# Kernel tuning notes

Hardware: AMD Instinct MI355X
Metric: run time of the kernel (lower is better)

Reference implementation:

```python
import math
import jax, jax.numpy as jnp
import numpy as np

DIM, NHEAD, TOPK = 1024, 16, 64
DK = DIM // NHEAD
HIDDEN = int(DIM * 8.0)
EPS = 1e-5


def setup_inputs() -> dict:
    key = jax.random.key(0)
    ks = jax.random.split(key, 12)
    B, T = 2, 2048
    s = 0.02
    return {
        "x": jax.random.normal(ks[0], (B, T, DIM), jnp.float32),
        "ln1_g": jnp.ones((DIM,), jnp.float32),
        "ln1_b": jnp.zeros((DIM,), jnp.float32),
        "w_qkv": jax.random.normal(ks[1], (DIM, 3 * DIM), jnp.float32) * s,
        "alpha_head": jnp.zeros((NHEAD,), jnp.float32),
        "w_out": jax.random.normal(ks[2], (DIM, DIM), jnp.float32) * s,
        "ln2_g": jnp.ones((DIM,), jnp.float32),
        "ln2_b": jnp.zeros((DIM,), jnp.float32),
        "w1": jax.random.normal(ks[3], (DIM, HIDDEN), jnp.float32) * s,
        "b1": jnp.zeros((HIDDEN,), jnp.float32),
        "w2": jax.random.normal(ks[4], (HIDDEN, DIM), jnp.float32) * s,
        "b2": jnp.zeros((DIM,), jnp.float32),
        "alpha": jnp.float32(0.5),
    }


def _layernorm(x, g, b):
    mu = jnp.mean(x, axis=-1, keepdims=True)
    var = jnp.var(x, axis=-1, keepdims=True)
    return (x - mu) * jax.lax.rsqrt(var + EPS) * g + b


def _adaptive_sparse_attn(xn, w_qkv, alpha_head, w_out):
    B, T, C = xn.shape
    qkv = xn @ w_qkv  # [B,T,3C]
    q, k, v = jnp.split(qkv, 3, axis=-1)
    def heads(t):
        return t.reshape(B, T, NHEAD, DK).transpose(0, 2, 1, 3)  # [B,H,T,dk]
    q, k, v = heads(q), heads(k), heads(v)
    attn = jnp.einsum("bhqd,bhkd->bhqk", q, k) / math.sqrt(DK)  # [B,H,T,T]
    dense = jnp.einsum("bhqk,bhkd->bhqd", jax.nn.softmax(attn, axis=-1), v)
    # top-k sparse branch (TOPK < T)
    _, idx = jax.lax.top_k(attn, TOPK)  # [B,H,T,TOPK]
    M = B * NHEAD * T
    keep = jnp.zeros((M, T), bool).at[jnp.arange(M)[:, None], idx.reshape(M, TOPK)].set(True)
    keep = keep.reshape(B, NHEAD, T, T)
    attn_sp = jnp.where(keep, attn, jnp.float32(-1e9))
    sparse = jnp.einsum("bhqk,bhkd->bhqd", jax.nn.softmax(attn_sp, axis=-1), v)
    gate = jax.nn.sigmoid(alpha_head)[None, :, None, None]
    out = gate * dense + (1.0 - gate) * sparse  # [B,H,T,dk]
    out = out.transpose(0, 2, 1, 3).reshape(B, T, C)
    return out @ w_out


def reference(x, ln1_g, ln1_b, w_qkv, alpha_head, w_out, ln2_g, ln2_b, w1, b1, w2, b2, alpha):
    # attention sub-block with learned residual scale alpha
    x = x + alpha * _adaptive_sparse_attn(_layernorm(x, ln1_g, ln1_b), w_qkv, alpha_head, w_out)
    # FFN (dropout in eval mode -> identity); exact GELU as torch default
    h = jax.nn.gelu(_layernorm(x, ln2_g, ln2_b) @ w1 + b1, approximate=False)
    x = x + alpha * (h @ w2 + b2)
    return x
```

## Files before the change

kernel.cpp:

```cpp
#include <hip/hip_runtime.h>
#include <math.h>

#define DIMC 1024
#define NHEADC 16
#define DKC 64
#define HIDC 8192
#define TSEQ 2048
#define BATCH 2
#define NROWS (BATCH*TSEQ)
#define EPSF 1e-5f

typedef __attribute__((ext_vector_type(8))) short short8;
typedef __attribute__((ext_vector_type(4))) float floatx4;

__device__ __forceinline__ ushort f2bf(float f){
  unsigned u = __float_as_uint(f);
  unsigned r = (u + 0x7FFFu + ((u>>16)&1u)) >> 16;
  return (ushort)r;
}
__device__ __forceinline__ float bf2f(ushort u){
  return __uint_as_float(((unsigned)u)<<16);
}
__device__ __forceinline__ floatx4 mfma16(short8 a, short8 b, floatx4 c){
  return __builtin_amdgcn_mfma_f32_16x16x32_bf16(a, b, c, 0, 0, 0);
}
__device__ __forceinline__ void gld_lds16(const void* g, void* l){
  __builtin_amdgcn_global_load_lds((const __attribute__((address_space(1))) unsigned*)g,
                                   (__attribute__((address_space(3))) unsigned*)l, 16, 0, 0);
}
__device__ __forceinline__ float wred_add(float v){
  #pragma unroll
  for (int o = 32; o > 0; o >>= 1) v += __shfl_xor(v, o, 64);
  return v;
}
__device__ __forceinline__ float wred_max(float v){
  #pragma unroll
  for (int o = 32; o > 0; o >>= 1) v = fmaxf(v, __shfl_xor(v, o, 64));
  return v;
}

__global__ __launch_bounds__(256)
void wconv_t(const float* __restrict__ W, ushort* __restrict__ WT, int K, int N)
{
  __shared__ float tile[32][33];
  const int t = threadIdx.x, tx = t & 31, ty = t >> 5;
  const int n0 = blockIdx.x * 32, k0 = blockIdx.y * 32;
  #pragma unroll
  for (int r = 0; r < 4; ++r)
    tile[ty + r*8][tx] = W[(size_t)(k0 + ty + r*8) * N + n0 + tx];
  __syncthreads();
  #pragma unroll
  for (int r = 0; r < 4; ++r)
    WT[(size_t)(n0 + ty + r*8) * K + k0 + tx] = f2bf(tile[tx][ty + r*8]);
}

__global__ __launch_bounds__(256)
void vtrans(const ushort* __restrict__ qkv, ushort* __restrict__ vT)
{
  const int d = threadIdx.x & 63, tp = threadIdx.x >> 6;
  const int bh = blockIdx.y; const int h = bh & 15, b = bh >> 4;
  const int t0 = blockIdx.x * 32 + tp * 8;
  const ushort* src = qkv + ((size_t)(b*TSEQ) + t0) * (3*DIMC) + 2*DIMC + h*DKC + d;
  ushort tmp[8];
  #pragma unroll
  for (int k = 0; k < 8; ++k) tmp[k] = src[(size_t)k * (3*DIMC)];
  *(short8*)&vT[((size_t)bh*DKC + d)*TSEQ + t0] = *(const short8*)tmp;
}

__global__ __launch_bounds__(256)
void ln_bf16(const float* __restrict__ x, const float* __restrict__ g,
             const float* __restrict__ b, ushort* __restrict__ y)
{
  __shared__ float red[8];
  const int row = blockIdx.x;
  const float* xr = x + (size_t)row * DIMC;
  const int c = threadIdx.x * 4;
  float4 v = *(const float4*)&xr[c];
  float s  = v.x + v.y + v.z + v.w;
  float ss = v.x*v.x + v.y*v.y + v.z*v.z + v.w*v.w;
  s = wred_add(s); ss = wred_add(ss);
  const int warp = threadIdx.x >> 6, lane = threadIdx.x & 63;
  if (lane == 0) { red[warp] = s; red[4+warp] = ss; }
  __syncthreads();
  s  = red[0] + red[1] + red[2] + red[3];
  ss = red[4] + red[5] + red[6] + red[7];
  const float mu  = s  * (1.f/DIMC);
  const float var = ss * (1.f/DIMC) - mu*mu;
  const float rr  = rsqrtf(var + EPSF);
  const float4 gv = *(const float4*)&g[c];
  const float4 bv = *(const float4*)&b[c];
  ushort4 o;
  o.x = f2bf((v.x-mu)*rr*gv.x + bv.x);
  o.y = f2bf((v.y-mu)*rr*gv.y + bv.y);
  o.z = f2bf((v.z-mu)*rr*gv.z + bv.z);
  o.w = f2bf((v.w-mu)*rr*gv.w + bv.w);
  *(ushort4*)&y[(size_t)row*DIMC + c] = o;
}

#define M_PLAIN 0
#define M_RES 1
#define M_BIAS_GELU 2
#define M_BIAS_RES 3

template<int MODE>
__global__ __launch_bounds__(256)
void gemm_bf16(const ushort* __restrict__ A, const ushort* __restrict__ BT,
               void* __restrict__ Cout, const int M, const int N, const int K,
               const float* __restrict__ bias, const float* __restrict__ res,
               const float* __restrict__ alphap)
{
  __shared__ __align__(16) ushort Al[4][128][8];
  __shared__ __align__(16) ushort Bl[4][128][8];
  const int t = threadIdx.x;
  const int lane = t & 63, warp = t >> 6;
  const int quad = lane >> 4, l16 = lane & 15;
  const int m0 = (warp & 1) * 64, n0 = (warp >> 1) * 64;
  const size_t row0 = (size_t)blockIdx.y * 128;
  const size_t col0 = (size_t)blockIdx.x * 128;

  const int c0 = t, c1 = t + 256;
  const int ar0 = c0 & 127, as0 = c0 >> 7;
  const int ar1 = c1 & 127, as1 = c1 >> 7;
  const ushort* pa0 = A  + (row0 + ar0) * (size_t)K + as0 * 8;
  const ushort* pa1 = A  + (row0 + ar1) * (size_t)K + as1 * 8;
  const ushort* pb0 = BT + (col0 + ar0) * (size_t)K + as0 * 8;
  const ushort* pb1 = BT + (col0 + ar1) * (size_t)K + as1 * 8;
  ushort* la0 = &Al[as0][ar0][0];
  ushort* la1 = &Al[as1][ar1][0];
  ushort* lb0 = &Bl[as0][ar0][0];
  ushort* lb1 = &Bl[as1][ar1][0];

  floatx4 acc[4][4];
  const floatx4 zf = {0.f, 0.f, 0.f, 0.f};
  #pragma unroll
  for (int i = 0; i < 4; ++i)
    #pragma unroll
    for (int j = 0; j < 4; ++j) acc[i][j] = zf;

  for (int k0 = 0; k0 < K; k0 += 32) {
    gld_lds16(pa0 + k0, la0);
    gld_lds16(pa1 + k0, la1);
    gld_lds16(pb0 + k0, lb0);
    gld_lds16(pb1 + k0, lb1);
    __syncthreads();
    short8 af[4], bfr[4];
    #pragma unroll
    for (int i = 0; i < 4; ++i) {
      af[i]  = *(const short8*)&Al[quad][m0 + i*16 + l16][0];
      bfr[i] = *(const short8*)&Bl[quad][n0 + i*16 + l16][0];
    }
    #pragma unroll
    for (int mt = 0; mt < 4; ++mt)
      #pragma unroll
      for (int nt = 0; nt < 4; ++nt)
        acc[mt][nt] = mfma16(af[mt], bfr[nt], acc[mt][nt]);
    __syncthreads();
  }

  float alpha = 0.f;
  if (MODE == M_RES || MODE == M_BIAS_RES) alpha = alphap[0];
  #pragma unroll
  for (int nt = 0; nt < 4; ++nt) {
    const size_t col = col0 + n0 + nt*16 + l16;
    float bv = 0.f;
    if (MODE == M_BIAS_GELU || MODE == M_BIAS_RES) bv = bias[col];
    #pragma unroll
    for (int mt = 0; mt < 4; ++mt) {
      const size_t r0 = row0 + m0 + mt*16 + quad*4;
      #pragma unroll
      for (int reg = 0; reg < 4; ++reg) {
        float v = acc[mt][nt][reg];
        if (MODE == M_BIAS_GELU || MODE == M_BIAS_RES) v += bv;
        if (MODE == M_BIAS_GELU) v = 0.5f*v*(1.f + erff(v*0.70710678118654752f));
        if (MODE == M_RES || MODE == M_BIAS_RES) v = res[(r0+reg)*(size_t)N + col] + alpha*v;
        if (MODE == M_PLAIN || MODE == M_BIAS_GELU)
          ((ushort*)Cout)[(r0+reg)*(size_t)N + col] = f2bf(v);
        else
          ((float*)Cout)[(r0+reg)*(size_t)N + col] = v;
      }
    }
  }
}

__device__ __forceinline__ int swzf(int q){ return ((q>>2) ^ q) & 7; }
__device__ __forceinline__ int sidx(int q, int j){
  return (q << 11) + ((((j >> 3) ^ swzf(q)) << 3) | (j & 7));
}

__global__ __launch_bounds__(512, 4)
void attn_mfma(const ushort* __restrict__ qkv, const ushort* __restrict__ vT,
               const float* __restrict__ alpha_head, ushort* __restrict__ att)
{
  __shared__ __align__(16) ushort S[16*2048];
  __shared__ float Ored[4][16*17];
  const int t = threadIdx.x;
  const int lane = t & 63, warp = t >> 6;
  const int quad = lane >> 4, l16 = lane & 15;
  const int blk = blockIdx.x;
  const int bh  = blk >> 7;
  const int q0  = (blk & 127) << 4;
  const int h = bh & (NHEADC-1), b = bh >> 4;
  const size_t rowbase = (size_t)b * TSEQ;
  const floatx4 zf = {0.f, 0.f, 0.f, 0.f};

  const ushort* Qp = qkv + (rowbase + q0 + l16) * (size_t)(3*DIMC) + h*DKC + quad*8;
  const short8 aq0 = *(const short8*)Qp;
  const short8 aq1 = *(const short8*)(Qp + 32);

  const int j0w = warp * 256;
  #pragma unroll 2
  for (int jt = 0; jt < 16; ++jt) {
    const int j = j0w + jt*16;
    const ushort* Kp = qkv + (rowbase + j + l16) * (size_t)(3*DIMC) + DIMC + h*DKC + quad*8;
    const short8 kb0 = *(const short8*)Kp;
    const short8 kb1 = *(const short8*)(Kp + 32);
    floatx4 c = mfma16(aq0, kb0, zf);
    c = mfma16(aq1, kb1, c);
    #pragma unroll
    for (int r = 0; r < 4; ++r)
      S[sidx(quad*4 + r, j + l16)] = f2bf(c[r] * 0.125f);
  }
  __syncthreads();

  const float L2E = 1.4426950408889634f;
  const float gate = 1.f / (1.f + __expf(-alpha_head[h]));
  for (int rr = 0; rr < 2; ++rr) {
    const int q = warp*2 + rr;
    const int sbase = q << 11;
    const int swq = swzf(q);
    unsigned key[32]; float ev[32];
    float mx = -3.0e38f;
    #pragma unroll
    for (int p = 0; p < 16; ++p) {
      const int j = 2*lane + 128*p;
      const int g = (j >> 3) ^ swq;
      const unsigned pr = *(const unsigned*)&S[sbase + (g << 3) + (j & 7)];
      const unsigned u0 = pr & 0xFFFFu, u1 = pr >> 16;
      key[2*p]   = (u0 & 0x8000u) ? ((~u0) & 0xFFFFu) : (u0 | 0x8000u);
      key[2*p+1] = (u1 & 0x8000u) ? ((~u1) & 0xFFFFu) : (u1 | 0x8000u);
      const float v0 = __uint_as_float(pr << 16);
      const float v1 = __uint_as_float(pr & 0xFFFF0000u);
      ev[2*p] = v0; ev[2*p+1] = v1;
      mx = fmaxf(mx, fmaxf(v0, v1));
    }
    mx = wred_max(mx);
    const float nc = -mx * L2E;
    float sum_all = 0.f;
    #pragma unroll
    for (int i = 0; i < 32; ++i) { ev[i] = exp2f(fmaf(ev[i], L2E, nc)); sum_all += ev[i]; }
    sum_all = wred_add(sum_all);

    unsigned prefix = 0u;
    for (int bit = 15; bit >= 0; --bit) {
      const unsigned cand = prefix | (1u << bit);
      int c = 0;
      #pragma unroll
      for (int i = 0; i < 32; ++i)
        c += __popcll(__ballot(key[i] >= cand));
      if (c >= 64) prefix = cand;
    }
    unsigned inmask = 0u;
    float sum_sp = 0.f;
    int c_gt = 0;
    #pragma unroll
    for (int i = 0; i < 32; ++i) {
      const bool gbit = key[i] > prefix;
      c_gt += __popcll(__ballot(gbit));
      if (gbit) { inmask |= (1u << i); sum_sp += ev[i]; }
    }
    const int need_eq = 64 - c_gt;
    int eqb = 0;
    const unsigned long long below = (1ULL << lane) - 1ULL;
    for (int p = 0; p < 16; ++p) {
      const bool e0 = (key[2*p]   == prefix);
      const bool e1 = (key[2*p+1] == prefix);
      const unsigned long long m0 = __ballot(e0);
      const unsigned long long m1 = __ballot(e1);
      if (m0 | m1) {
        const int r0 = eqb + __popcll(m0 & below) + __popcll(m1 & below);
        const int r1 = r0 + (e0 ? 1 : 0);
        if (e0 && r0 < need_eq) { inmask |= (1u << (2*p));   sum_sp += ev[2*p]; }
        if (e1 && r1 < need_eq) { inmask |= (1u << (2*p+1)); sum_sp += ev[2*p+1]; }
        eqb += __popcll(m0) + __popcll(m1);
      }
    }
    sum_sp = wred_add(sum_sp);

    const float cd  = gate / sum_all;
    const float cdc = cd + (1.f - gate) / sum_sp;
    #pragma unroll
    for (int p = 0; p < 16; ++p) {
      const float w0 = ev[2*p]   * (((inmask >> (2*p))   & 1u) ? cdc : cd);
      const float w1 = ev[2*p+1] * (((inmask >> (2*p+1)) & 1u) ? cdc : cd);
      const int j = 2*lane + 128*p;
      const int g = (j >> 3) ^ swq;
      *(unsigned*)&S[sbase + (g << 3) + (j & 7)] =
          (unsigned)f2bf(w0) | ((unsigned)f2bf(w1) << 16);
    }
  }
  __syncthreads();

  const int n0  = (warp & 3) * 16;
  const int kt0 = (warp >> 2) * 32;
  floatx4 o = zf, o2 = zf;
  const ushort* Vb = vT + ((size_t)bh*DKC + n0 + l16) * TSEQ + quad*8;
  #pragma unroll 2
  for (int tt = 0; tt < 32; tt += 2) {
    const int kt = kt0 + tt;
    const short8 a0 = *(const short8*)&S[sidx(l16, kt*32 + quad*8)];
    const short8 vb0 = *(const short8*)(Vb + (size_t)kt*32);
    const short8 a1 = *(const short8*)&S[sidx(l16, (kt+1)*32 + quad*8)];
    const short8 vb1 = *(const short8*)(Vb + (size_t)(kt+1)*32);
    o  = mfma16(a0, vb0, o);
    o2 = mfma16(a1, vb1, o2);
  }
  o = o + o2;
  if (warp >= 4) {
    #pragma unroll
    for (int r = 0; r < 4; ++r) Ored[warp-4][(quad*4+r)*17 + l16] = o[r];
  }
  __syncthreads();
  if (warp < 4) {
    #pragma unroll
    for (int r = 0; r < 4; ++r) {
      const float v = o[r] + Ored[warp][(quad*4+r)*17 + l16];
      att[(rowbase + q0 + quad*4 + r) * (size_t)DIMC + h*DKC + n0 + l16] = f2bf(v);
    }
  }
}

extern "C" void kernel_launch(void* const* d_in, const int* in_sizes, int n_in,
                              void* d_out, int out_size, void* d_ws, size_t ws_size,
                              hipStream_t stream)
{
  const float* x          = (const float*)d_in[0];
  const float* ln1_g      = (const float*)d_in[1];
  const float* ln1_b      = (const float*)d_in[2];
  const float* w_qkv      = (const float*)d_in[3];
  const float* alpha_head = (const float*)d_in[4];
  const float* w_out      = (const float*)d_in[5];
  const float* ln2_g      = (const float*)d_in[6];
  const float* ln2_b      = (const float*)d_in[7];
  const float* w1         = (const float*)d_in[8];
  const float* b1         = (const float*)d_in[9];
  const float* w2         = (const float*)d_in[10];
  const float* b2         = (const float*)d_in[11];
  const float* alphap     = (const float*)d_in[12];
  float* out = (float*)d_out;

  char* ws = (char*)d_ws;
  ushort* wT_qkv = (ushort*)(ws);
  ushort* wT_out = (ushort*)(ws + 6291456);
  ushort* wT_1   = (ushort*)(ws + 8388608);
  ushort* wT_2   = (ushort*)(ws + 25165824);
  ushort* xn     = (ushort*)(ws + 41943040);
  ushort* qkv    = (ushort*)(ws + 50331648);
  ushort* attb   = (ushort*)(ws + 75497472);
  float*  x2     = (float*) (ws + 83886080);
  ushort* hbuf   = (ushort*)(ws + 100663296);
  ushort* vT     = (ushort*)(ws + 167772160);

  wconv_t<<<dim3(3072/32, 1024/32), 256, 0, stream>>>(w_qkv, wT_qkv, 1024, 3072);
  wconv_t<<<dim3(1024/32, 1024/32), 256, 0, stream>>>(w_out, wT_out, 1024, 1024);
  wconv_t<<<dim3(8192/32, 1024/32), 256, 0, stream>>>(w1,    wT_1,   1024, 8192);
  wconv_t<<<dim3(1024/32, 8192/32), 256, 0, stream>>>(w2,    wT_2,   8192, 1024);

  ln_bf16<<<NROWS, 256, 0, stream>>>(x, ln1_g, ln1_b, xn);
  gemm_bf16<M_PLAIN><<<dim3(3*DIMC/128, NROWS/128), 256, 0, stream>>>(
      xn, wT_qkv, qkv, NROWS, 3*DIMC, DIMC, nullptr, nullptr, nullptr);
  vtrans<<<dim3(64, 32), 256, 0, stream>>>(qkv, vT);
  attn_mfma<<<4096, 512, 0, stream>>>(qkv, vT, alpha_head, attb);
  gemm_bf16<M_RES><<<dim3(DIMC/128, NROWS/128), 256, 0, stream>>>(
      attb, wT_out, x2, NROWS, DIMC, DIMC, nullptr, x, alphap);
  ln_bf16<<<NROWS, 256, 0, stream>>>(x2, ln2_g, ln2_b, xn);
  gemm_bf16<M_BIAS_GELU><<<dim3(HIDC/128, NROWS/128), 256, 0, stream>>>(
      xn, wT_1, hbuf, NROWS, HIDC, DIMC, b1, nullptr, nullptr);
  gemm_bf16<M_BIAS_RES><<<dim3(DIMC/128, NROWS/128), 256, 0, stream>>>(
      hbuf, wT_2, out, NROWS, DIMC, HIDC, b2, x2, alphap);
}
```

Baseline: 1.018 ms.

## Double attention block to 1024 threads, one query row per warp

Widens the attention block from 8 to 16 warps so each warp computes half as many score tiles, runs the softmax/top-k selection on a single query row instead of two, and covers a quarter of the keys in the PV product. Partial outputs from the four key quarters are reduced through a larger shared buffer. The 1/sqrt(dk) scale is moved out of the score store and folded into the exp2 constant, so scores are stored unscaled in bf16, which slightly changes rounding. The cost is a 1024-thread block with tighter register limits per thread and one more level of partial-sum reduction.

```diff
diff --git a/kernel.cpp b/kernel.cpp
--- a/kernel.cpp
+++ b/kernel.cpp
@@ -17,9 +17,6 @@
   unsigned u = __float_as_uint(f);
   unsigned r = (u + 0x7FFFu + ((u>>16)&1u)) >> 16;
   return (ushort)r;
-}
-__device__ __forceinline__ float bf2f(ushort u){
-  return __uint_as_float(((unsigned)u)<<16);
 }
 __device__ __forceinline__ floatx4 mfma16(short8 a, short8 b, floatx4 c){
   return __builtin_amdgcn_mfma_f32_16x16x32_bf16(a, b, c, 0, 0, 0);
@@ -187,12 +184,12 @@
   return (q << 11) + ((((j >> 3) ^ swzf(q)) << 3) | (j & 7));
 }
 
-__global__ __launch_bounds__(512, 4)
+__global__ __launch_bounds__(1024, 8)
 void attn_mfma(const ushort* __restrict__ qkv, const ushort* __restrict__ vT,
                const float* __restrict__ alpha_head, ushort* __restrict__ att)
 {
   __shared__ __align__(16) ushort S[16*2048];
-  __shared__ float Ored[4][16*17];
+  __shared__ float Ored[3][4][16*17];
   const int t = threadIdx.x;
   const int lane = t & 63, warp = t >> 6;
   const int quad = lane >> 4, l16 = lane & 15;
@@ -207,9 +204,9 @@
   const short8 aq0 = *(const short8*)Qp;
   const short8 aq1 = *(const short8*)(Qp + 32);
 
-  const int j0w = warp * 256;
-  #pragma unroll 2
-  for (int jt = 0; jt < 16; ++jt) {
+  const int j0w = warp * 128;
+  #pragma unroll
+  for (int jt = 0; jt < 8; ++jt) {
     const int j = j0w + jt*16;
     const ushort* Kp = qkv + (rowbase + j + l16) * (size_t)(3*DIMC) + DIMC + h*DKC + quad*8;
     const short8 kb0 = *(const short8*)Kp;
@@ -218,14 +215,14 @@
     c = mfma16(aq1, kb1, c);
     #pragma unroll
     for (int r = 0; r < 4; ++r)
-      S[sidx(quad*4 + r, j + l16)] = f2bf(c[r] * 0.125f);
-  }
-  __syncthreads();
-
-  const float L2E = 1.4426950408889634f;
+      S[sidx(quad*4 + r, j + l16)] = f2bf(c[r]);
+  }
+  __syncthreads();
+
+  const float SC2 = 0.125f * 1.4426950408889634f;
   const float gate = 1.f / (1.f + __expf(-alpha_head[h]));
-  for (int rr = 0; rr < 2; ++rr) {
-    const int q = warp*2 + rr;
+  {
+    const int q = warp;
     const int sbase = q << 11;
     const int swq = swzf(q);
     unsigned key[32]; float ev[32];
@@ -244,10 +241,10 @@
       mx = fmaxf(mx, fmaxf(v0, v1));
     }
     mx = wred_max(mx);
-    const float nc = -mx * L2E;
+    const float nc = -mx * SC2;
     float sum_all = 0.f;
     #pragma unroll
-    for (int i = 0; i < 32; ++i) { ev[i] = exp2f(fmaf(ev[i], L2E, nc)); sum_all += ev[i]; }
+    for (int i = 0; i < 32; ++i) { ev[i] = exp2f(fmaf(ev[i], SC2, nc)); sum_all += ev[i]; }
     sum_all = wred_add(sum_all);
 
     unsigned prefix = 0u;
@@ -300,12 +297,13 @@
   }
   __syncthreads();
 
-  const int n0  = (warp & 3) * 16;
-  const int kt0 = (warp >> 2) * 32;
+  const int ng = warp & 3, kq = warp >> 2;
+  const int n0  = ng * 16;
+  const int kt0 = kq * 16;
   floatx4 o = zf, o2 = zf;
   const ushort* Vb = vT + ((size_t)bh*DKC + n0 + l16) * TSEQ + quad*8;
   #pragma unroll 2
-  for (int tt = 0; tt < 32; tt += 2) {
+  for (int tt = 0; tt < 16; tt += 2) {
     const int kt = kt0 + tt;
     const short8 a0 = *(const short8*)&S[sidx(l16, kt*32 + quad*8)];
     const short8 vb0 = *(const short8*)(Vb + (size_t)kt*32);
@@ -315,15 +313,16 @@
     o2 = mfma16(a1, vb1, o2);
   }
   o = o + o2;
-  if (warp >= 4) {
-    #pragma unroll
-    for (int r = 0; r < 4; ++r) Ored[warp-4][(quad*4+r)*17 + l16] = o[r];
-  }
-  __syncthreads();
-  if (warp < 4) {
+  if (kq > 0) {
+    #pragma unroll
+    for (int r = 0; r < 4; ++r) Ored[kq-1][ng][(quad*4+r)*17 + l16] = o[r];
+  }
+  __syncthreads();
+  if (kq == 0) {
     #pragma unroll
     for (int r = 0; r < 4; ++r) {
-      const float v = o[r] + Ored[warp][(quad*4+r)*17 + l16];
+      const int ri = (quad*4+r)*17 + l16;
+      const float v = o[r] + Ored[0][ng][ri] + Ored[1][ng][ri] + Ored[2][ng][ri];
       att[(rowbase + q0 + quad*4 + r) * (size_t)DIMC + h*DKC + n0 + l16] = f2bf(v);
     }
   }
@@ -369,7 +368,7 @@
   gemm_bf16<M_PLAIN><<<dim3(3*DIMC/128, NROWS/128), 256, 0, stream>>>(
       xn, wT_qkv, qkv, NROWS, 3*DIMC, DIMC, nullptr, nullptr, nullptr);
   vtrans<<<dim3(64, 32), 256, 0, stream>>>(qkv, vT);
-  attn_mfma<<<4096, 512, 0, stream>>>(qkv, vT, alpha_head, attb);
+  attn_mfma<<<4096, 1024, 0, stream>>>(qkv, vT, alpha_head, attb);
   gemm_bf16<M_RES><<<dim3(DIMC/128, NROWS/128), 256, 0, stream>>>(
       attb, wT_out, x2, NROWS, DIMC, DIMC, nullptr, x, alphap);
   ln_bf16<<<NROWS, 256, 0, stream>>>(x2, ln2_g, ln2_b, xn);
```

Result: slower. 1.223 ms (+20.1%).
